# Optimization experiments

Hardware: AMD Instinct MI355X
Metric: run time of the kernel (lower is better)

## Reference

```python
import jax, jax.numpy as jnp
import numpy as np

NEG_SLOPE = 0.01  # F.leaky_relu default


def _unfold3(x):
    # x: [B,C,H,W] -> [B,C,9,H,W] of 3x3 neighborhoods (zero pad 1)
    B, C, H, W = x.shape
    xp = jnp.pad(x, ((0, 0), (0, 0), (1, 1), (1, 1)))
    return jnp.stack([xp[:, :, i:i + H, j:j + W] for i in range(3) for j in range(3)], axis=2)


def _resize_bilinear(img, oh, ow):
    # torch F.interpolate mode='bilinear', align_corners=False, antialias=False
    B, C, H, W = img.shape
    if oh == H and ow == W:
        return img
    def coords(out, inn):
        c = jnp.maximum((jnp.arange(out, dtype=jnp.float32) + 0.5) * (inn / out) - 0.5, 0.0)
        i0 = jnp.floor(c).astype(jnp.int32)
        i1 = jnp.minimum(i0 + 1, inn - 1)
        w = c - i0.astype(jnp.float32)
        return i0, i1, w
    i0, i1, wh = coords(oh, H)
    row = img[:, :, i0, :] * (1.0 - wh)[None, None, :, None] + img[:, :, i1, :] * wh[None, None, :, None]
    j0, j1, ww = coords(ow, W)
    return row[:, :, :, j0] * (1.0 - ww) + row[:, :, :, j1] * ww


def _up2_nearest(x):
    # F.interpolate scale_factor=2 (default mode='nearest')
    return jnp.repeat(jnp.repeat(x, 2, axis=2), 2, axis=3)


def _leaky(x):
    return jnp.where(x >= 0, x, NEG_SLOPE * x)


def _pac_conv(x, guide, w):
    # PacConv2d (gaussian kernel, k=3, stride=1, pad=1, bias=False)
    g_unf = _unfold3(guide)                      # [B,Cg,9,H,W]
    diff = g_unf - guide[:, :, None]             # f_j - f_i
    kern = jnp.exp(-0.5 * jnp.sum(diff * diff, axis=1))  # [B,9,H,W]
    x_unf = _unfold3(x)                          # [B,Ci,9,H,W]
    wk = w.reshape(w.shape[0], w.shape[1], 9)    # [Co,Ci,9]
    return jnp.einsum('oik,bikhw,bkhw->bohw', wk, x_unf, kern)


def setup_inputs() -> dict:
    key = jax.random.key(0)
    ks = jax.random.split(key, 8)
    B, Cx, Hx, Wx = 4, 384, 32, 32
    Hg = Wg = 512
    x = jax.random.normal(ks[0], (B, Cx, Hx, Wx), dtype=jnp.float32)
    guide = jax.random.uniform(ks[1], (B, 3, Hg, Wg), dtype=jnp.float32)
    lin_w = jax.random.normal(ks[2], (16, 384, 1, 1), dtype=jnp.float32) * 0.05
    lin_b = jax.random.normal(ks[3], (16,), dtype=jnp.float32) * 0.05
    chans = [16, 4, 4, 4, 1]
    w0 = jax.random.normal(ks[4], (chans[1], chans[0], 3, 3), dtype=jnp.float32) * 0.1
    w1 = jax.random.normal(ks[5], (chans[2], chans[1], 3, 3), dtype=jnp.float32) * 0.1
    w2 = jax.random.normal(ks[6], (chans[3], chans[2], 3, 3), dtype=jnp.float32) * 0.1
    w3 = jax.random.normal(ks[7], (chans[4], chans[3], 3, 3), dtype=jnp.float32) * 0.1
    return {"x": x, "guide": guide, "lin_w": lin_w, "lin_b": lin_b,
            "w0": w0, "w1": w1, "w2": w2, "w3": w3}


def reference(x, guide, lin_w, lin_b, w0, w1, w2, w3):
    # crop guide to multiple of 16 (module uses shape[-1] for both dims)
    s = (guide.shape[-1] // 16) * 16
    guide = guide[..., :s, :s]
    # 1x1 conv + leaky relu
    x = jnp.einsum('oi,bihw->bohw', lin_w[:, :, 0, 0], x) + lin_b[None, :, None, None]
    x = _leaky(x)
    ws = [w0, w1, w2, w3]
    n = len(ws)
    Hg, Wg = guide.shape[2], guide.shape[3]
    for i in range(n):
        f = 2 ** (n - 1 - i)
        g = _resize_bilinear(guide, Hg // f, Wg // f)
        x = _up2_nearest(x)
        x = _pac_conv(x, g, ws[i])
        if i < n - 1:
            x = _leaky(x)
    return jax.nn.sigmoid(x)
```

## Files before the change

kernel.cpp:

```cpp
#include <hip/hip_runtime.h>
#include <math.h>

#define NEG_SLOPE 0.01f

__global__ void linear_leaky_kernel(const float* __restrict__ x,
                                    const float* __restrict__ w,
                                    const float* __restrict__ b,
                                    float* __restrict__ out) {
    int idx = blockIdx.x * blockDim.x + threadIdx.x;
    int hw = idx & 1023;
    int co = (idx >> 10) & 15;
    int bb = idx >> 14;
    const float* xp = x + bb * 384 * 1024 + hw;
    const float* wp = w + co * 384;
    float acc = b[co];
#pragma unroll 8
    for (int ci = 0; ci < 384; ++ci)
        acc = fmaf(wp[ci], xp[ci * 1024], acc);
    out[idx] = acc >= 0.f ? acc : NEG_SLOPE * acc;
}

__global__ void resize_kernel(const float* __restrict__ g,
                              float* __restrict__ out, int R) {
    int idx = blockIdx.x * blockDim.x + threadIdx.x;
    int total = 4 * 3 * R * R;
    if (idx >= total) return;
    int w = idx % R;
    int h = (idx / R) % R;
    int bc = idx / (R * R);
    float scale = 512.0f / (float)R;
    float ch = fmaxf((h + 0.5f) * scale - 0.5f, 0.f);
    float cw = fmaxf((w + 0.5f) * scale - 0.5f, 0.f);
    int h0 = (int)ch;
    int w0 = (int)cw;
    int h1 = min(h0 + 1, 511);
    int w1 = min(w0 + 1, 511);
    float fh = ch - (float)h0;
    float fw = cw - (float)w0;
    const float* gp = g + (size_t)bc * 512 * 512;
    float v00 = gp[h0 * 512 + w0];
    float v01 = gp[h0 * 512 + w1];
    float v10 = gp[h1 * 512 + w0];
    float v11 = gp[h1 * 512 + w1];
    float top = v00 + (v01 - v00) * fw;
    float bot = v10 + (v11 - v10) * fw;
    out[idx] = top + (bot - top) * fh;
}

template <int Ci, int Co, int ACT>
__global__ void pac_conv_kernel(const float* __restrict__ x,
                                const float* __restrict__ g,
                                const float* __restrict__ wk,
                                float* __restrict__ out,
                                int H, int W) {
    __shared__ float sw[Co * Ci * 9];
    for (int i = threadIdx.x; i < Co * Ci * 9; i += blockDim.x) sw[i] = wk[i];
    __syncthreads();

    int idx = blockIdx.x * blockDim.x + threadIdx.x;
    int total = 4 * H * W;
    if (idx >= total) return;
    int w = idx % W;
    int h = (idx / W) % H;
    int b = idx / (H * W);
    int Hh = H >> 1, Wh = W >> 1;
    int HW = H * W;

    const float* gb = g + (size_t)b * 3 * HW;
    float gc0 = gb[h * W + w];
    float gc1 = gb[HW + h * W + w];
    float gc2 = gb[2 * HW + h * W + w];

    float acc[Co];
#pragma unroll
    for (int co = 0; co < Co; ++co) acc[co] = 0.f;

    const float* xb = x + (size_t)b * Ci * Hh * Wh;

#pragma unroll
    for (int t = 0; t < 9; ++t) {
        int dh = t / 3 - 1, dw = t % 3 - 1;
        int hh = h + dh, ww = w + dw;
        if (hh < 0 || hh >= H || ww < 0 || ww >= W) continue;
        float d0 = gb[hh * W + ww] - gc0;
        float d1 = gb[HW + hh * W + ww] - gc1;
        float d2 = gb[2 * HW + hh * W + ww] - gc2;
        float k = __expf(-0.5f * (d0 * d0 + d1 * d1 + d2 * d2));
        const float* xp = xb + (hh >> 1) * Wh + (ww >> 1);
#pragma unroll
        for (int ci = 0; ci < Ci; ++ci) {
            float xv = xp[ci * Hh * Wh] * k;
#pragma unroll
            for (int co = 0; co < Co; ++co)
                acc[co] = fmaf(sw[(co * Ci + ci) * 9 + t], xv, acc[co]);
        }
    }

#pragma unroll
    for (int co = 0; co < Co; ++co) {
        float v = acc[co];
        if (ACT == 0) {
            v = v >= 0.f ? v : NEG_SLOPE * v;
        } else {
            v = 1.0f / (1.0f + __expf(-v));
        }
        out[((size_t)(b * Co + co) * HW) + h * W + w] = v;
    }
}

extern "C" void kernel_launch(void* const* d_in, const int* in_sizes, int n_in,
                              void* d_out, int out_size, void* d_ws, size_t ws_size,
                              hipStream_t stream) {
    const float* x     = (const float*)d_in[0];
    const float* guide = (const float*)d_in[1];
    const float* lin_w = (const float*)d_in[2];
    const float* lin_b = (const float*)d_in[3];
    const float* w0    = (const float*)d_in[4];
    const float* w1    = (const float*)d_in[5];
    const float* w2    = (const float*)d_in[6];
    const float* w3    = (const float*)d_in[7];
    float* out = (float*)d_out;

    float* ws = (float*)d_ws;
    float* x16  = ws;
    float* g64  = x16  + 65536;
    float* x0   = g64  + 49152;
    float* g128 = x0   + 65536;
    float* x1   = g128 + 196608;
    float* g256 = x1   + 262144;
    float* x2   = g256 + 786432;

    const int B = 256;

    linear_leaky_kernel<<<65536 / B, B, 0, stream>>>(x, lin_w, lin_b, x16);

    resize_kernel<<<(49152 + B - 1) / B, B, 0, stream>>>(guide, g64, 64);
    pac_conv_kernel<16, 4, 0><<<(4 * 64 * 64) / B, B, 0, stream>>>(x16, g64, w0, x0, 64, 64);

    resize_kernel<<<(196608 + B - 1) / B, B, 0, stream>>>(guide, g128, 128);
    pac_conv_kernel<4, 4, 0><<<(4 * 128 * 128) / B, B, 0, stream>>>(x0, g128, w1, x1, 128, 128);

    resize_kernel<<<(786432 + B - 1) / B, B, 0, stream>>>(guide, g256, 256);
    pac_conv_kernel<4, 4, 0><<<(4 * 256 * 256) / B, B, 0, stream>>>(x1, g256, w2, x2, 256, 256);

    pac_conv_kernel<4, 1, 1><<<(4 * 512 * 512) / B, B, 0, stream>>>(x2, guide, w3, out, 512, 512);
}
```

Before: 142.5 us.

## Fuse all stages into one cooperative persistent kernel with grid syncs

Replaces seven separate kernel launches with a single cooperative kernel of 256 blocks that runs the linear layer, the guide resizes and the four PAC convolutions, separated by grid-wide barriers. It loads all conv weights into shared memory once and uses grid-stride loops for the larger stages. This is meant to remove per-launch overhead and the gaps between launches. The trade-off is low occupancy, with one block per CU on a fixed grid, plus the cost of grid-wide syncs. The linear stage also splits its reduction into four independent accumulators.

```diff
diff --git a/kernel.cpp b/kernel.cpp
--- a/kernel.cpp
+++ b/kernel.cpp
@@ -1,82 +1,47 @@
 #include <hip/hip_runtime.h>
+#include <hip/hip_cooperative_groups.h>
 #include <math.h>
+
+namespace cg = cooperative_groups;
 
 #define NEG_SLOPE 0.01f
 
-__global__ void linear_leaky_kernel(const float* __restrict__ x,
-                                    const float* __restrict__ w,
-                                    const float* __restrict__ b,
-                                    float* __restrict__ out) {
-    int idx = blockIdx.x * blockDim.x + threadIdx.x;
-    int hw = idx & 1023;
-    int co = (idx >> 10) & 15;
-    int bb = idx >> 14;
-    const float* xp = x + bb * 384 * 1024 + hw;
-    const float* wp = w + co * 384;
-    float acc = b[co];
-#pragma unroll 8
-    for (int ci = 0; ci < 384; ++ci)
-        acc = fmaf(wp[ci], xp[ci * 1024], acc);
-    out[idx] = acc >= 0.f ? acc : NEG_SLOPE * acc;
-}
-
-__global__ void resize_kernel(const float* __restrict__ g,
-                              float* __restrict__ out, int R) {
-    int idx = blockIdx.x * blockDim.x + threadIdx.x;
-    int total = 4 * 3 * R * R;
-    if (idx >= total) return;
+__device__ inline void resize_px(const float* __restrict__ g, float* __restrict__ out,
+                                 int R, int idx) {
     int w = idx % R;
     int h = (idx / R) % R;
     int bc = idx / (R * R);
     float scale = 512.0f / (float)R;
     float ch = fmaxf((h + 0.5f) * scale - 0.5f, 0.f);
     float cw = fmaxf((w + 0.5f) * scale - 0.5f, 0.f);
-    int h0 = (int)ch;
-    int w0 = (int)cw;
-    int h1 = min(h0 + 1, 511);
-    int w1 = min(w0 + 1, 511);
-    float fh = ch - (float)h0;
-    float fw = cw - (float)w0;
-    const float* gp = g + (size_t)bc * 512 * 512;
-    float v00 = gp[h0 * 512 + w0];
-    float v01 = gp[h0 * 512 + w1];
-    float v10 = gp[h1 * 512 + w0];
-    float v11 = gp[h1 * 512 + w1];
+    int h0 = (int)ch, w0 = (int)cw;
+    int h1 = min(h0 + 1, 511), w1 = min(w0 + 1, 511);
+    float fh = ch - (float)h0, fw = cw - (float)w0;
+    const float* gp = g + (size_t)bc * (512 * 512);
+    float v00 = gp[h0 * 512 + w0], v01 = gp[h0 * 512 + w1];
+    float v10 = gp[h1 * 512 + w0], v11 = gp[h1 * 512 + w1];
     float top = v00 + (v01 - v00) * fw;
     float bot = v10 + (v11 - v10) * fw;
     out[idx] = top + (bot - top) * fh;
 }
 
 template <int Ci, int Co, int ACT>
-__global__ void pac_conv_kernel(const float* __restrict__ x,
-                                const float* __restrict__ g,
-                                const float* __restrict__ wk,
-                                float* __restrict__ out,
-                                int H, int W) {
-    __shared__ float sw[Co * Ci * 9];
-    for (int i = threadIdx.x; i < Co * Ci * 9; i += blockDim.x) sw[i] = wk[i];
-    __syncthreads();
-
-    int idx = blockIdx.x * blockDim.x + threadIdx.x;
-    int total = 4 * H * W;
-    if (idx >= total) return;
+__device__ inline void pac_px(const float* __restrict__ x, const float* __restrict__ g,
+                              const float* __restrict__ sw, float* __restrict__ out,
+                              int idx, int H, int W) {
     int w = idx % W;
     int h = (idx / W) % H;
     int b = idx / (H * W);
     int Hh = H >> 1, Wh = W >> 1;
     int HW = H * W;
-
     const float* gb = g + (size_t)b * 3 * HW;
     float gc0 = gb[h * W + w];
     float gc1 = gb[HW + h * W + w];
     float gc2 = gb[2 * HW + h * W + w];
-
     float acc[Co];
 #pragma unroll
     for (int co = 0; co < Co; ++co) acc[co] = 0.f;
-
     const float* xb = x + (size_t)b * Ci * Hh * Wh;
-
 #pragma unroll
     for (int t = 0; t < 9; ++t) {
         int dh = t / 3 - 1, dw = t % 3 - 1;
@@ -95,17 +60,72 @@
                 acc[co] = fmaf(sw[(co * Ci + ci) * 9 + t], xv, acc[co]);
         }
     }
-
 #pragma unroll
     for (int co = 0; co < Co; ++co) {
         float v = acc[co];
-        if (ACT == 0) {
-            v = v >= 0.f ? v : NEG_SLOPE * v;
-        } else {
-            v = 1.0f / (1.0f + __expf(-v));
+        if (ACT == 0) v = v >= 0.f ? v : NEG_SLOPE * v;
+        else         v = 1.0f / (1.0f + __expf(-v));
+        out[(size_t)(b * Co + co) * HW + h * W + w] = v;
+    }
+}
+
+__global__ void __launch_bounds__(256)
+pacnet_fused(const float* __restrict__ x, const float* __restrict__ guide,
+             const float* __restrict__ lin_w, const float* __restrict__ lin_b,
+             const float* __restrict__ w0, const float* __restrict__ w1,
+             const float* __restrict__ w2, const float* __restrict__ w3,
+             float* __restrict__ out, float* __restrict__ ws) {
+    float* x16  = ws;
+    float* g64  = x16 + 65536;
+    float* x0   = g64 + 49152;
+    float* g128 = x0 + 65536;
+    float* x1   = g128 + 196608;
+    float* g256 = x1 + 262144;
+    float* x2   = g256 + 786432;
+
+    __shared__ float sw[576 + 144 + 144 + 36];
+    float* sw0 = sw;
+    float* sw1 = sw0 + 576;
+    float* sw2 = sw1 + 144;
+    float* sw3 = sw2 + 144;
+    for (int i = threadIdx.x; i < 576; i += 256) sw0[i] = w0[i];
+    for (int i = threadIdx.x; i < 144; i += 256) sw1[i] = w1[i];
+    for (int i = threadIdx.x; i < 144; i += 256) sw2[i] = w2[i];
+    for (int i = threadIdx.x; i < 36;  i += 256) sw3[i] = w3[i];
+
+    cg::grid_group grid = cg::this_grid();
+    const int tid = blockIdx.x * blockDim.x + threadIdx.x;
+    const int T = gridDim.x * blockDim.x;
+
+    {
+        int hw = tid & 1023, co = (tid >> 10) & 15, bb = tid >> 14;
+        const float* xp = x + bb * 384 * 1024 + hw;
+        const float* wp = lin_w + co * 384;
+        float a0 = 0.f, a1 = 0.f, a2 = 0.f, a3 = 0.f;
+        for (int ci = 0; ci < 384; ci += 4) {
+            a0 = fmaf(wp[ci],     xp[(ci)     * 1024], a0);
+            a1 = fmaf(wp[ci + 1], xp[(ci + 1) * 1024], a1);
+            a2 = fmaf(wp[ci + 2], xp[(ci + 2) * 1024], a2);
+            a3 = fmaf(wp[ci + 3], xp[(ci + 3) * 1024], a3);
         }
-        out[((size_t)(b * Co + co) * HW) + h * W + w] = v;
+        float acc = lin_b[co] + ((a0 + a1) + (a2 + a3));
+        x16[tid] = acc >= 0.f ? acc : NEG_SLOPE * acc;
     }
+    for (int i = tid; i < 49152;  i += T) resize_px(guide, g64,  64,  i);
+    for (int i = tid; i < 196608; i += T) resize_px(guide, g128, 128, i);
+    for (int i = tid; i < 786432; i += T) resize_px(guide, g256, 256, i);
+    grid.sync();
+
+    if (tid < 16384) pac_px<16, 4, 0>(x16, g64, sw0, x0, tid, 64, 64);
+    grid.sync();
+
+    for (int i = tid; i < 65536; i += T) pac_px<4, 4, 0>(x0, g128, sw1, x1, i, 128, 128);
+    grid.sync();
+
+    for (int i = tid; i < 262144; i += T) pac_px<4, 4, 0>(x1, g256, sw2, x2, i, 256, 256);
+    grid.sync();
+
+    for (int i = tid; i < 1048576; i += T) pac_px<4, 1, 1>(x2, guide, sw3, out, i, 512, 512);
 }
 
 extern "C" void kernel_launch(void* const* d_in, const int* in_sizes, int n_in,
@@ -120,28 +140,11 @@
     const float* w2    = (const float*)d_in[6];
     const float* w3    = (const float*)d_in[7];
     float* out = (float*)d_out;
+    float* wsf = (float*)d_ws;
 
-    float* ws = (float*)d_ws;
-    float* x16  = ws;
-    float* g64  = x16  + 65536;
-    float* x0   = g64  + 49152;
-    float* g128 = x0   + 65536;
-    float* x1   = g128 + 196608;
-    float* g256 = x1   + 262144;
-    float* x2   = g256 + 786432;
-
-    const int B = 256;
-
-    linear_leaky_kernel<<<65536 / B, B, 0, stream>>>(x, lin_w, lin_b, x16);
-
-    resize_kernel<<<(49152 + B - 1) / B, B, 0, stream>>>(guide, g64, 64);
-    pac_conv_kernel<16, 4, 0><<<(4 * 64 * 64) / B, B, 0, stream>>>(x16, g64, w0, x0, 64, 64);
-
-    resize_kernel<<<(196608 + B - 1) / B, B, 0, stream>>>(guide, g128, 128);
-    pac_conv_kernel<4, 4, 0><<<(4 * 128 * 128) / B, B, 0, stream>>>(x0, g128, w1, x1, 128, 128);
-
-    resize_kernel<<<(786432 + B - 1) / B, B, 0, stream>>>(guide, g256, 256);
-    pac_conv_kernel<4, 4, 0><<<(4 * 256 * 256) / B, B, 0, stream>>>(x1, g256, w2, x2, 256, 256);
-
-    pac_conv_kernel<4, 1, 1><<<(4 * 512 * 512) / B, B, 0, stream>>>(x2, guide, w3, out, 512, 512);
+    void* args[] = {(void*)&x, (void*)&guide, (void*)&lin_w, (void*)&lin_b,
+                    (void*)&w0, (void*)&w1, (void*)&w2, (void*)&w3,
+                    (void*)&out, (void*)&wsf};
+    dim3 grid(256), block(256);
+    hipLaunchCooperativeKernel((void*)pacnet_fused, grid, block, args, 0, stream);
 }
```

Measured after the change: 315.9 us. 122% more time.
